# Kernel tuning notes

Measured on AMD Instinct MI355X. Metric: run time of the kernel, lower is better.

Reference implementation:

```python
import jax, jax.numpy as jnp
import numpy as np

# Instant-NGP / tcnn hash grid encoding constants (from init_kwargs)
L = 16           # n_levels
F = 2            # n_features_per_level
T = 2 ** 15      # hashmap size per level
DIM = 3
BASE = 16.0      # base_resolution
FINEST = 512.0   # finest_resolution
RANGE = 1.0
B = (FINEST / BASE) ** (1.0 / (L - 1))  # per_level_scale
N_POINTS = 500000
# tcnn spatial hash primes (first dim uses 1)
PRIMES = jnp.array([1, 2654435761, 805459861], dtype=jnp.uint32)


def setup_inputs() -> dict:
    key = jax.random.key(0)
    k1, k2 = jax.random.split(key)
    x = jax.random.uniform(k1, (N_POINTS, DIM), dtype=jnp.float32)  # points in [0,1)
    table = jax.random.normal(k2, (L, T, F), dtype=jnp.float32) * 1e-4  # tcnn-style tiny init
    return {"x": x, "table": table}


def reference(x, table):
    # wrapper: map from [-range, range] to [0, 1]
    xn = (x + RANGE) / (2.0 * RANGE)                       # [N, 3]
    n = xn.shape[0]
    # per-level grid scale (tcnn: scale = base * b^l - 1)
    scales = BASE * (B ** jnp.arange(L, dtype=jnp.float32)) - 1.0  # [L]
    pos = xn[:, None, :] * scales[None, :, None] + 0.5     # [N, L, 3]
    pos_floor = jnp.floor(pos)
    frac = pos - pos_floor                                  # [N, L, 3]
    grid = pos_floor.astype(jnp.uint32)                    # [N, L, 3]
    # 8 cube corners as binary offsets
    corners = jnp.array([[(c >> d) & 1 for d in range(DIM)] for c in range(2 ** DIM)],
                        dtype=jnp.uint32)                   # [8, 3]
    coords = grid[:, :, None, :] + corners[None, None, :, :]  # [N, L, 8, 3] uint32
    h = coords * PRIMES                                     # uint32 wraps (modular mult)
    idx = (h[..., 0] ^ h[..., 1] ^ h[..., 2]) & jnp.uint32(T - 1)  # [N, L, 8]
    # gather per-level features: [N, L, 8, F]
    feats = table[jnp.arange(L)[None, :, None], idx]
    # trilinear interpolation weights
    cf = corners.astype(jnp.float32)                        # [8, 3]
    w = jnp.prod(jnp.where(cf[None, None, :, :] == 1.0,
                           frac[:, :, None, :],
                           1.0 - frac[:, :, None, :]), axis=-1)  # [N, L, 8]
    out = jnp.einsum('nlc,nlcf->nlf', w, feats)             # [N, L, F]
    return out.reshape(n, L * F)
```

## Files before the change

### kernel.cpp

```cpp
#include <hip/hip_runtime.h>
#include <hip/hip_fp16.h>
#include <stdint.h>


constexpr int      kL  = 16;
constexpr int      kT  = 32768;
constexpr uint32_t kM  = kT - 1;
constexpr uint32_t kP1 = 2654435761u;
constexpr uint32_t kP2 = 805459861u;
constexpr int      kNC = 16;
constexpr int      kBT = 1024;

typedef float f32x2 __attribute__((ext_vector_type(2)));

__device__ __constant__ float c_scales[kL] = {
    15.0f,
    19.158736798317972f,
    24.398416831491190f,
    31.0f,
    39.317473596635944f,
    49.796833662982380f,
    63.0f,
    79.634947193271890f,
    100.59366732596477f,
    127.0f,
    160.26989438654378f,
    202.18733465192953f,
    255.0f,
    321.53978877308750f,
    405.37466930385903f,
    511.0f
};

__global__ __launch_bounds__(kBT, 4) void hashgrid_fwd(
    const float*  __restrict__ x,
    const float2* __restrict__ table,
    f32x2*        __restrict__ out,
    int n_points, int chunk_sz)
{
    __shared__ uint32_t ltab[kT];

    int bid = blockIdx.x;
    int l   = bid >> 4;
    int c   = bid & 15;

    const float4* tsrc4 = reinterpret_cast<const float4*>(table + (size_t)l * kT);
    for (int e = threadIdx.x; e < kT / 2; e += kBT) {
        float4 q = tsrc4[e];
        uint2 pp;
        pp.x = ((uint32_t)__half_as_ushort(__float2half_rn(q.y)) << 16)
             |  (uint32_t)__half_as_ushort(__float2half_rn(q.x));
        pp.y = ((uint32_t)__half_as_ushort(__float2half_rn(q.w)) << 16)
             |  (uint32_t)__half_as_ushort(__float2half_rn(q.z));
        *reinterpret_cast<uint2*>(&ltab[e * 2]) = pp;
    }
    __syncthreads();

    float s = c_scales[l];
    int base = c * chunk_sz;
    int lim  = min(base + chunk_sz, n_points);

    for (int n0 = base + (int)threadIdx.x; n0 < lim; n0 += 2 * kBT) {
        int nn[2];
        nn[0] = n0;
        int nB = n0 + kBT;
        bool hasB = nB < lim;
        nn[1] = hasB ? nB : n0;

        uint32_t idx[2][8];
        float    w[2][8];

#pragma unroll
        for (int p = 0; p < 2; ++p) {
            int n = nn[p];
            float x0 = x[n * 3 + 0];
            float x1 = x[n * 3 + 1];
            float x2 = x[n * 3 + 2];

            float p0 = fmaf((x0 + 1.0f) * 0.5f, s, 0.5f);
            float p1 = fmaf((x1 + 1.0f) * 0.5f, s, 0.5f);
            float p2 = fmaf((x2 + 1.0f) * 0.5f, s, 0.5f);

            float fl0 = floorf(p0), fl1 = floorf(p1), fl2 = floorf(p2);
            float fr0 = p0 - fl0,   fr1 = p1 - fl1,   fr2 = p2 - fl2;

            uint32_t g0 = (uint32_t)(int)fl0;
            uint32_t g1 = (uint32_t)(int)fl1;
            uint32_t g2 = (uint32_t)(int)fl2;

            uint32_t hx0 = g0;        uint32_t hx1 = g0 + 1u;
            uint32_t hy0 = g1 * kP1;  uint32_t hy1 = hy0 + kP1;
            uint32_t hz0 = g2 * kP2;  uint32_t hz1 = hz0 + kP2;

            float wy0 = 1.0f - fr1, wz0 = 1.0f - fr2;
            float wx0 = 1.0f - fr0;

            float wyz[4];
            wyz[0] = wy0 * wz0;
            wyz[1] = fr1 * wz0;
            wyz[2] = wy0 * fr2;
            wyz[3] = fr1 * fr2;

            uint32_t hyz[4];
            hyz[0] = hy0 ^ hz0;
            hyz[1] = hy1 ^ hz0;
            hyz[2] = hy0 ^ hz1;
            hyz[3] = hy1 ^ hz1;

#pragma unroll
            for (int cc = 0; cc < 8; ++cc) {
                uint32_t hx = (cc & 1) ? hx1 : hx0;
                idx[p][cc] = (hx ^ hyz[cc >> 1]) & kM;
                w[p][cc]   = ((cc & 1) ? fr0 : wx0) * wyz[cc >> 1];
            }
        }

        uint32_t e[2][8];
#pragma unroll
        for (int p = 0; p < 2; ++p)
#pragma unroll
            for (int cc = 0; cc < 8; ++cc)
                e[p][cc] = ltab[idx[p][cc]];

        f32x2 r[2];
#pragma unroll
        for (int p = 0; p < 2; ++p) {
            float acc_x = 0.0f, acc_y = 0.0f;
#pragma unroll
            for (int cc = 0; cc < 8; ++cc) {
                __half2 h = *reinterpret_cast<__half2*>(&e[p][cc]);
                acc_x = fmaf(w[p][cc], __low2float(h),  acc_x);
                acc_y = fmaf(w[p][cc], __high2float(h), acc_y);
            }
            r[p].x = acc_x; r[p].y = acc_y;
        }

        out[(size_t)nn[0] * kL + l] = r[0];
        if (hasB) out[(size_t)nn[1] * kL + l] = r[1];
    }
}

extern "C" void kernel_launch(void* const* d_in, const int* in_sizes, int n_in,
                              void* d_out, int out_size, void* d_ws, size_t ws_size,
                              hipStream_t stream) {
    const float*  x     = (const float*)d_in[0];
    const float2* table = (const float2*)d_in[1];
    f32x2*        out   = (f32x2*)d_out;

    int n_points = in_sizes[0] / 3;
    int chunk_sz = (n_points + kNC - 1) / kNC;
    int blocks   = kL * kNC;

    hashgrid_fwd<<<blocks, kBT, 0, stream>>>(x, table, out, n_points, chunk_sz);
}
```

Baseline: 49.31 us.

## Software-pipeline LDS gathers across point batches and accumulate in packed half

Restructures the per-point loop into a two-stage software pipeline. The LDS gathers and the x loads for the next point are issued before the current point's results are consumed, with sched_barriers keeping the order in place. This is meant to hide LDS gather latency and global load latency. It also switches the trilinear accumulation from fp32 FMAs to packed half2 FMAs, which cuts ALU work but loses accuracy in the accumulation.

```diff
diff --git a/kernel.cpp b/kernel.cpp
--- a/kernel.cpp
+++ b/kernel.cpp
@@ -32,6 +32,63 @@
     511.0f
 };
 
+__device__ __forceinline__ void load3(float (&v)[3], const float* __restrict__ x, int n) {
+    v[0] = x[n * 3 + 0];
+    v[1] = x[n * 3 + 1];
+    v[2] = x[n * 3 + 2];
+}
+
+__device__ __forceinline__ void issue8(
+    const uint32_t* __restrict__ ltab, float s, const float (&xv)[3],
+    uint32_t (&buf)[8], float (&w)[8])
+{
+    float p0 = fmaf((xv[0] + 1.0f) * 0.5f, s, 0.5f);
+    float p1 = fmaf((xv[1] + 1.0f) * 0.5f, s, 0.5f);
+    float p2 = fmaf((xv[2] + 1.0f) * 0.5f, s, 0.5f);
+
+    float fl0 = floorf(p0), fl1 = floorf(p1), fl2 = floorf(p2);
+    float fr0 = p0 - fl0,   fr1 = p1 - fl1,   fr2 = p2 - fl2;
+
+    uint32_t g0 = (uint32_t)(int)fl0;
+    uint32_t g1 = (uint32_t)(int)fl1;
+    uint32_t g2 = (uint32_t)(int)fl2;
+
+    uint32_t hx0 = g0;        uint32_t hx1 = g0 + 1u;
+    uint32_t hy0 = g1 * kP1;  uint32_t hy1 = hy0 + kP1;
+    uint32_t hz0 = g2 * kP2;  uint32_t hz1 = hz0 + kP2;
+
+    float wy0 = 1.0f - fr1, wz0 = 1.0f - fr2;
+    float wx0 = 1.0f - fr0;
+
+    uint32_t hyz[4];
+    float    wyz[4];
+    hyz[0] = hy0 ^ hz0;  wyz[0] = wy0 * wz0;
+    hyz[1] = hy1 ^ hz0;  wyz[1] = fr1 * wz0;
+    hyz[2] = hy0 ^ hz1;  wyz[2] = wy0 * fr2;
+    hyz[3] = hy1 ^ hz1;  wyz[3] = fr1 * fr2;
+
+#pragma unroll
+    for (int cc = 0; cc < 8; ++cc) {
+        uint32_t hx = (cc & 1) ? hx1 : hx0;
+        uint32_t idx = (hx ^ hyz[cc >> 1]) & kM;
+        w[cc]   = ((cc & 1) ? fr0 : wx0) * wyz[cc >> 1];
+        buf[cc] = ltab[idx];
+    }
+}
+
+__device__ __forceinline__ f32x2 consume8(const uint32_t (&buf)[8], const float (&w)[8]) {
+    __half2 acc = __float2half2_rn(0.0f);
+#pragma unroll
+    for (int cc = 0; cc < 8; ++cc) {
+        __half2 h = *reinterpret_cast<const __half2*>(&buf[cc]);
+        acc = __hfma2(__float2half2_rn(w[cc]), h, acc);
+    }
+    f32x2 r;
+    r.x = __low2float(acc);
+    r.y = __high2float(acc);
+    return r;
+}
+
 __global__ __launch_bounds__(kBT, 4) void hashgrid_fwd(
     const float*  __restrict__ x,
     const float2* __restrict__ table,
@@ -56,87 +113,40 @@
     }
     __syncthreads();
 
-    float s = c_scales[l];
-    int base = c * chunk_sz;
-    int lim  = min(base + chunk_sz, n_points);
+    float s    = c_scales[l];
+    int   base = c * chunk_sz;
+    int   lim  = min(base + chunk_sz, n_points);
+    int   nmax = lim - 1;
+    int   iters = (chunk_sz + kBT - 1) / kBT;
 
-    for (int n0 = base + (int)threadIdx.x; n0 < lim; n0 += 2 * kBT) {
-        int nn[2];
-        nn[0] = n0;
-        int nB = n0 + kBT;
-        bool hasB = nB < lim;
-        nn[1] = hasB ? nB : n0;
+    uint32_t bufA[8], bufB[8];
+    float    wA[8],  wB[8];
+    float    xA[3],  xB[3];
 
-        uint32_t idx[2][8];
-        float    w[2][8];
+    int nA = base + (int)threadIdx.x;
+    load3(xA, x, min(nA, nmax));
+    load3(xB, x, min(nA + kBT, nmax));
 
-#pragma unroll
-        for (int p = 0; p < 2; ++p) {
-            int n = nn[p];
-            float x0 = x[n * 3 + 0];
-            float x1 = x[n * 3 + 1];
-            float x2 = x[n * 3 + 2];
+    issue8(ltab, s, xA, bufA, wA);
+    __builtin_amdgcn_sched_barrier(0);
 
-            float p0 = fmaf((x0 + 1.0f) * 0.5f, s, 0.5f);
-            float p1 = fmaf((x1 + 1.0f) * 0.5f, s, 0.5f);
-            float p2 = fmaf((x2 + 1.0f) * 0.5f, s, 0.5f);
-
-            float fl0 = floorf(p0), fl1 = floorf(p1), fl2 = floorf(p2);
-            float fr0 = p0 - fl0,   fr1 = p1 - fl1,   fr2 = p2 - fl2;
-
-            uint32_t g0 = (uint32_t)(int)fl0;
-            uint32_t g1 = (uint32_t)(int)fl1;
-            uint32_t g2 = (uint32_t)(int)fl2;
-
-            uint32_t hx0 = g0;        uint32_t hx1 = g0 + 1u;
-            uint32_t hy0 = g1 * kP1;  uint32_t hy1 = hy0 + kP1;
-            uint32_t hz0 = g2 * kP2;  uint32_t hz1 = hz0 + kP2;
-
-            float wy0 = 1.0f - fr1, wz0 = 1.0f - fr2;
-            float wx0 = 1.0f - fr0;
-
-            float wyz[4];
-            wyz[0] = wy0 * wz0;
-            wyz[1] = fr1 * wz0;
-            wyz[2] = wy0 * fr2;
-            wyz[3] = fr1 * fr2;
-
-            uint32_t hyz[4];
-            hyz[0] = hy0 ^ hz0;
-            hyz[1] = hy1 ^ hz0;
-            hyz[2] = hy0 ^ hz1;
-            hyz[3] = hy1 ^ hz1;
-
-#pragma unroll
-            for (int cc = 0; cc < 8; ++cc) {
-                uint32_t hx = (cc & 1) ? hx1 : hx0;
-                idx[p][cc] = (hx ^ hyz[cc >> 1]) & kM;
-                w[p][cc]   = ((cc & 1) ? fr0 : wx0) * wyz[cc >> 1];
-            }
+    for (int it = 0; it < iters; it += 2) {
+        if (it + 1 < iters) issue8(ltab, s, xB, bufB, wB);
+        load3(xA, x, min(nA + 2 * kBT, nmax));
+        __builtin_amdgcn_sched_barrier(0);
+        {
+            f32x2 r = consume8(bufA, wA);
+            if (nA < lim) out[(size_t)nA * kL + l] = r;
         }
-
-        uint32_t e[2][8];
-#pragma unroll
-        for (int p = 0; p < 2; ++p)
-#pragma unroll
-            for (int cc = 0; cc < 8; ++cc)
-                e[p][cc] = ltab[idx[p][cc]];
-
-        f32x2 r[2];
-#pragma unroll
-        for (int p = 0; p < 2; ++p) {
-            float acc_x = 0.0f, acc_y = 0.0f;
-#pragma unroll
-            for (int cc = 0; cc < 8; ++cc) {
-                __half2 h = *reinterpret_cast<__half2*>(&e[p][cc]);
-                acc_x = fmaf(w[p][cc], __low2float(h),  acc_x);
-                acc_y = fmaf(w[p][cc], __high2float(h), acc_y);
-            }
-            r[p].x = acc_x; r[p].y = acc_y;
+        if (it + 2 < iters) issue8(ltab, s, xA, bufA, wA);
+        load3(xB, x, min(nA + 3 * kBT, nmax));
+        __builtin_amdgcn_sched_barrier(0);
+        if (it + 1 < iters) {
+            f32x2 r = consume8(bufB, wB);
+            int nB = nA + kBT;
+            if (nB < lim) out[(size_t)nB * kL + l] = r;
         }
-
-        out[(size_t)nn[0] * kL + l] = r[0];
-        if (hasB) out[(size_t)nn[1] * kL + l] = r[1];
+        nA += 2 * kBT;
     }
 }
 
```

New measurement: 49.78 us. About the same (+0.9%).

## Pair coarse and fine levels per block, process two levels sequentially

Applied to the files above, without the earlier changes.

Each block now handles a pair of levels (l and 15-l) in two phases, reloading the level table into LDS between phases, with point chunks doubled to 32. The goal is to balance per-block work and cache behaviour between coarse and fine levels. The two-points-per-iteration interleave is dropped in favour of one point per thread per iteration, and the position affine transform is folded into a single FMA. The block count stays the same, but each block now does two serialized table loads separated by syncs, and memory-level parallelism per thread drops.

```diff
diff --git a/kernel.cpp b/kernel.cpp
--- a/kernel.cpp
+++ b/kernel.cpp
@@ -8,7 +8,7 @@
 constexpr uint32_t kM  = kT - 1;
 constexpr uint32_t kP1 = 2654435761u;
 constexpr uint32_t kP2 = 805459861u;
-constexpr int      kNC = 16;
+constexpr int      kNC = 32;
 constexpr int      kBT = 1024;
 
 typedef float f32x2 __attribute__((ext_vector_type(2)));
@@ -41,45 +41,43 @@
     __shared__ uint32_t ltab[kT];
 
     int bid = blockIdx.x;
-    int l   = bid >> 4;
-    int c   = bid & 15;
+    int p   = bid >> 5;
+    int c   = bid & 31;
 
-    const float4* tsrc4 = reinterpret_cast<const float4*>(table + (size_t)l * kT);
-    for (int e = threadIdx.x; e < kT / 2; e += kBT) {
-        float4 q = tsrc4[e];
-        uint2 pp;
-        pp.x = ((uint32_t)__half_as_ushort(__float2half_rn(q.y)) << 16)
-             |  (uint32_t)__half_as_ushort(__float2half_rn(q.x));
-        pp.y = ((uint32_t)__half_as_ushort(__float2half_rn(q.w)) << 16)
-             |  (uint32_t)__half_as_ushort(__float2half_rn(q.z));
-        *reinterpret_cast<uint2*>(&ltab[e * 2]) = pp;
-    }
-    __syncthreads();
-
-    float s = c_scales[l];
+    int tid  = (int)threadIdx.x;
     int base = c * chunk_sz;
     int lim  = min(base + chunk_sz, n_points);
 
-    for (int n0 = base + (int)threadIdx.x; n0 < lim; n0 += 2 * kBT) {
-        int nn[2];
-        nn[0] = n0;
-        int nB = n0 + kBT;
-        bool hasB = nB < lim;
-        nn[1] = hasB ? nB : n0;
+#pragma unroll
+    for (int phase = 0; phase < 2; ++phase) {
+        int l = (phase == 0) ? p : (kL - 1 - p);
 
-        uint32_t idx[2][8];
-        float    w[2][8];
+        __syncthreads();
 
-#pragma unroll
-        for (int p = 0; p < 2; ++p) {
-            int n = nn[p];
+        const float4* tsrc4 = reinterpret_cast<const float4*>(table + (size_t)l * kT);
+        for (int e = tid; e < kT / 2; e += kBT) {
+            float4 q = tsrc4[e];
+            uint2 pp;
+            pp.x = ((uint32_t)__half_as_ushort(__float2half_rn(q.y)) << 16)
+                 |  (uint32_t)__half_as_ushort(__float2half_rn(q.x));
+            pp.y = ((uint32_t)__half_as_ushort(__float2half_rn(q.w)) << 16)
+                 |  (uint32_t)__half_as_ushort(__float2half_rn(q.z));
+            *reinterpret_cast<uint2*>(&ltab[e * 2]) = pp;
+        }
+        __syncthreads();
+
+        float s = c_scales[l];
+        float A = s * 0.5f;
+        float C = fmaf(s, 0.5f, 0.5f);
+
+        for (int n = base + tid; n < lim; n += kBT) {
             float x0 = x[n * 3 + 0];
             float x1 = x[n * 3 + 1];
             float x2 = x[n * 3 + 2];
 
-            float p0 = fmaf((x0 + 1.0f) * 0.5f, s, 0.5f);
-            float p1 = fmaf((x1 + 1.0f) * 0.5f, s, 0.5f);
-            float p2 = fmaf((x2 + 1.0f) * 0.5f, s, 0.5f);
+            float p0 = fmaf(x0, A, C);
+            float p1 = fmaf(x1, A, C);
+            float p2 = fmaf(x2, A, C);
 
             float fl0 = floorf(p0), fl1 = floorf(p1), fl2 = floorf(p2);
             float fr0 = p0 - fl0,   fr1 = p1 - fl1,   fr2 = p2 - fl2;
@@ -88,55 +86,48 @@
             uint32_t g1 = (uint32_t)(int)fl1;
             uint32_t g2 = (uint32_t)(int)fl2;
 
-            uint32_t hx0 = g0;        uint32_t hx1 = g0 + 1u;
+            uint32_t g0p = g0 + 1u;
             uint32_t hy0 = g1 * kP1;  uint32_t hy1 = hy0 + kP1;
             uint32_t hz0 = g2 * kP2;  uint32_t hz1 = hz0 + kP2;
 
-            float wy0 = 1.0f - fr1, wz0 = 1.0f - fr2;
+            uint32_t hyz0 = hy0 ^ hz0;
+            uint32_t hyz1 = hy1 ^ hz0;
+            uint32_t hyz2 = hy0 ^ hz1;
+            uint32_t hyz3 = hy1 ^ hz1;
+
+            uint32_t e0 = ltab[(g0  ^ hyz0) & kM];
+            uint32_t e1 = ltab[(g0p ^ hyz0) & kM];
+            uint32_t e2 = ltab[(g0  ^ hyz1) & kM];
+            uint32_t e3 = ltab[(g0p ^ hyz1) & kM];
+            uint32_t e4 = ltab[(g0  ^ hyz2) & kM];
+            uint32_t e5 = ltab[(g0p ^ hyz2) & kM];
+            uint32_t e6 = ltab[(g0  ^ hyz3) & kM];
+            uint32_t e7 = ltab[(g0p ^ hyz3) & kM];
+
             float wx0 = 1.0f - fr0;
+            float wy0 = 1.0f - fr1;
+            float wz0 = 1.0f - fr2;
+            float wyz0 = wy0 * wz0;
+            float wyz1 = fr1 * wz0;
+            float wyz2 = wy0 * fr2;
+            float wyz3 = fr1 * fr2;
 
-            float wyz[4];
-            wyz[0] = wy0 * wz0;
-            wyz[1] = fr1 * wz0;
-            wyz[2] = wy0 * fr2;
-            wyz[3] = fr1 * fr2;
-
-            uint32_t hyz[4];
-            hyz[0] = hy0 ^ hz0;
-            hyz[1] = hy1 ^ hz0;
-            hyz[2] = hy0 ^ hz1;
-            hyz[3] = hy1 ^ hz1;
-
+            float acc_x = 0.0f, acc_y = 0.0f;
+            const uint32_t ee[8] = {e0, e1, e2, e3, e4, e5, e6, e7};
+            const float    wf[8] = {wx0 * wyz0, fr0 * wyz0,
+                                    wx0 * wyz1, fr0 * wyz1,
+                                    wx0 * wyz2, fr0 * wyz2,
+                                    wx0 * wyz3, fr0 * wyz3};
 #pragma unroll
             for (int cc = 0; cc < 8; ++cc) {
-                uint32_t hx = (cc & 1) ? hx1 : hx0;
-                idx[p][cc] = (hx ^ hyz[cc >> 1]) & kM;
-                w[p][cc]   = ((cc & 1) ? fr0 : wx0) * wyz[cc >> 1];
+                __half2 h = *reinterpret_cast<const __half2*>(&ee[cc]);
+                acc_x = fmaf(wf[cc], __low2float(h),  acc_x);
+                acc_y = fmaf(wf[cc], __high2float(h), acc_y);
             }
+
+            f32x2 r; r.x = acc_x; r.y = acc_y;
+            out[(size_t)n * kL + l] = r;
         }
-
-        uint32_t e[2][8];
-#pragma unroll
-        for (int p = 0; p < 2; ++p)
-#pragma unroll
-            for (int cc = 0; cc < 8; ++cc)
-                e[p][cc] = ltab[idx[p][cc]];
-
-        f32x2 r[2];
-#pragma unroll
-        for (int p = 0; p < 2; ++p) {
-            float acc_x = 0.0f, acc_y = 0.0f;
-#pragma unroll
-            for (int cc = 0; cc < 8; ++cc) {
-                __half2 h = *reinterpret_cast<__half2*>(&e[p][cc]);
-                acc_x = fmaf(w[p][cc], __low2float(h),  acc_x);
-                acc_y = fmaf(w[p][cc], __high2float(h), acc_y);
-            }
-            r[p].x = acc_x; r[p].y = acc_y;
-        }
-
-        out[(size_t)nn[0] * kL + l] = r[0];
-        if (hasB) out[(size_t)nn[1] * kL + l] = r[1];
     }
 }
 
@@ -149,7 +140,7 @@
 
     int n_points = in_sizes[0] / 3;
     int chunk_sz = (n_points + kNC - 1) / kNC;
-    int blocks   = kL * kNC;
+    int blocks   = (kL / 2) * kNC;
 
     hashgrid_fwd<<<blocks, kBT, 0, stream>>>(x, table, out, n_points, chunk_sz);
 }
```

After: 51.87 us. 1.05x slower.
